# Optimization experiments

Measured on AMD Instinct MI355X. Metric: run time of the kernel, lower is better.

The kernel has to match this reference:

```python
import jax, jax.numpy as jnp
import numpy as np
from jax import lax

B, T, S = 32, 64, 400
H, E, EMB, V = 512, 1024, 256, 32000


def setup_inputs() -> dict:
    key = jax.random.key(0)
    ks = jax.random.split(key, 16)
    w = lambda k, shape: jax.random.normal(k, shape, dtype=jnp.float32) * 0.05
    return {
        "target": jax.random.randint(ks[0], (B, T), 0, V),
        "h0": jax.random.normal(ks[1], (B, H), dtype=jnp.float32),
        "c0": jax.random.normal(ks[2], (B, H), dtype=jnp.float32),
        "enc_outs": jax.random.normal(ks[3], (S, B, E), dtype=jnp.float32),
        "attn_mask": jnp.ones((B, S), dtype=jnp.int32),
        "emb": w(ks[4], (V, EMB)),
        "W_ih": w(ks[5], (4 * H, EMB)),
        "b_ih": w(ks[6], (4 * H,)),
        "W_hh": w(ks[7], (4 * H, H)),
        "b_hh": w(ks[8], (4 * H,)),
        "W_attn": w(ks[9], (H, E)),
        "b_attn": w(ks[10], (H,)),
        "W_concat": w(ks[11], (H, E + H)),
        "b_concat": w(ks[12], (H,)),
        "W_out": w(ks[13], (V, H)),
        "b_out": w(ks[14], (V,)),
    }


def reference(target, h0, c0, enc_outs, attn_mask, emb, W_ih, b_ih, W_hh, b_hh,
              W_attn, b_attn, W_concat, b_concat, W_out, b_out):
    # Precompute attention keys projection once: [S, B, H]
    keys_proj = jnp.einsum("sbe,he->sbh", enc_outs, W_attn) + b_attn
    masked = attn_mask == 0  # [B, S]
    x_seq = emb[target].transpose(1, 0, 2)  # [T, B, EMB]

    def step(carry, x_t):
        h, c = carry
        # LSTMCell (torch gate order: i, f, g, o)
        gates = x_t @ W_ih.T + b_ih + h @ W_hh.T + b_hh  # [B, 4H]
        i, f, g, o = jnp.split(gates, 4, axis=1)
        c = jax.nn.sigmoid(f) * c + jax.nn.sigmoid(i) * jnp.tanh(g)
        h = jax.nn.sigmoid(o) * jnp.tanh(c)
        # additive-style attention: sum over hidden of query*key_proj
        scores = jnp.einsum("bh,sbh->bs", h, keys_proj)  # [B, S]
        scores = jnp.where(masked, jnp.float32(-1e18), scores)
        a = jax.nn.softmax(scores, axis=1)
        ctx = jnp.einsum("bs,sbe->be", a, enc_outs)  # [B, E]
        cat = jnp.tanh(jnp.concatenate([ctx, h], axis=1) @ W_concat.T + b_concat)
        logit = jax.nn.log_softmax(cat @ W_out.T + b_out, axis=-1)  # [B, V]
        return (h, c), logit

    (_, _), logits = lax.scan(step, (h0, c0), x_seq)  # [T, B, V]
    return logits.transpose(1, 0, 2)  # [B, T, V]
```

## Files before the change

kernel.cpp:

```cpp
#include <hip/hip_runtime.h>
#include <hip/hip_bf16.h>
#include <hip/hip_fp16.h>

#define B_ 32
#define T_ 64
#define S_ 400
#define H_ 512
#define E_ 1024
#define EMB_ 256
#define V_ 32000

typedef _Float16 f16;
typedef _Float16 half8 __attribute__((ext_vector_type(8)));
typedef float f32x4 __attribute__((ext_vector_type(4)));
typedef float f32x16 __attribute__((ext_vector_type(16)));
typedef unsigned uint4v __attribute__((ext_vector_type(4)));

__device__ __forceinline__ void gl_lds16(const void* g, void* l) {
  __builtin_amdgcn_global_load_lds(
      (const __attribute__((address_space(1))) void*)g,
      (__attribute__((address_space(3))) void*)l, 16, 0, 0);
}

__device__ __forceinline__ float sigmoidf_(float x) { return 1.f / (1.f + expf(-x)); }

__device__ __forceinline__ uint4v load_b128_sys(const void* p) {
  uint4v r;
  asm volatile("global_load_dwordx4 %0, %1, off sc0 sc1" : "=v"(r) : "v"(p) : "memory");
  return r;
}
__device__ __forceinline__ void store_b128_sys(void* p, uint4v v) {
  asm volatile("global_store_dwordx4 %0, %1, off sc0 sc1" :: "v"(p), "v"(v) : "memory");
}

__global__ __launch_bounds__(256) void cvt_f16_kernel(const float* __restrict__ src,
                                                      f16* __restrict__ dst, int n2) {
  int i = blockIdx.x * 256 + threadIdx.x;
  if (i >= n2) return;
  float2 v = reinterpret_cast<const float2*>(src)[i];
  union { f16 h[2]; unsigned u; } o;
  o.h[0] = (f16)v.x; o.h[1] = (f16)v.y;
  reinterpret_cast<unsigned*>(dst)[i] = o.u;
}

__global__ __launch_bounds__(256) void gather_x_kernel(const int* __restrict__ target,
                                                       const float* __restrict__ emb,
                                                       f16* __restrict__ xin) {
  int r = blockIdx.x;
  int t = r >> 5, b = r & 31;
  int tok = target[b * T_ + t];
  xin[(size_t)r * EMB_ + threadIdx.x] = (f16)emb[(size_t)tok * EMB_ + threadIdx.x];
}

__global__ __launch_bounds__(256) void prep_kernel(const float* __restrict__ b_ih,
                                                   const float* __restrict__ b_hh,
                                                   float* __restrict__ biasperm,
                                                   const float* __restrict__ Whh,
                                                   f16* __restrict__ Wperm,
                                                   const float* __restrict__ Wih,
                                                   f16* __restrict__ Wihp,
                                                   const float* __restrict__ h0,
                                                   f16* __restrict__ hbuf) {
  int idx = blockIdx.x * 256 + threadIdx.x;
  if (idx < 4 * H_) {
    int j = idx >> 2, gg = idx & 3;
    biasperm[idx] = b_ih[gg * H_ + j] + b_hh[gg * H_ + j];
  }
  if (idx < B_ * H_) hbuf[idx] = (f16)h0[idx];
  if (idx < T_ * B_ * H_ / 8) {
    uint4v p = {0xFFFFFFFFu, 0xFFFFFFFFu, 0xFFFFFFFFu, 0xFFFFFFFFu};
    reinterpret_cast<uint4v*>(reinterpret_cast<char*>(hbuf) + (size_t)B_ * H_ * 2)[idx] = p;
  }
  {
    int j = idx >> 9, k = idx & 511;
#pragma unroll
    for (int gg = 0; gg < 4; ++gg)
      Wperm[((size_t)(j * 4 + gg)) * H_ + k] = (f16)Whh[((size_t)(gg * H_ + j)) * H_ + k];
  }
  if (idx < H_ * EMB_) {
    int j = idx >> 8, k = idx & 255;
#pragma unroll
    for (int gg = 0; gg < 4; ++gg)
      Wihp[((size_t)(j * 4 + gg)) * EMB_ + k] = (f16)Wih[((size_t)(gg * H_ + j)) * EMB_ + k];
  }
}

template <int OUTK, bool DO_TANH>
__global__ __launch_bounds__(256) void gemm_bt_kernel(const f16* __restrict__ A,
                                                      const f16* __restrict__ W,
                                                      const float* __restrict__ bias,
                                                      void* __restrict__ outp,
                                                      int M, int N, int K) {
  __shared__ __align__(16) char As[128 * 64];
  __shared__ __align__(16) char Bs[128 * 64];
  const int tid = threadIdx.x;
  const int lane = tid & 63, wave = tid >> 6;
  const int wr = (wave >> 1) * 64, wc = (wave & 1) * 64;
  const int fr = lane & 15, fq = lane >> 4;
  const int row0 = blockIdx.x * 128, col0 = blockIdx.y * 128;

  f32x4 acc[4][4];
#pragma unroll
  for (int i = 0; i < 4; ++i)
#pragma unroll
    for (int j = 0; j < 4; ++j) acc[i][j] = {0.f, 0.f, 0.f, 0.f};

  for (int k0 = 0; k0 < K; k0 += 32) {
    __syncthreads();
#pragma unroll
    for (int i = 0; i < 2; ++i) {
      int o = tid * 16 + i * 4096;
      int r = o >> 6, kk = (o & 63) >> 1;
      gl_lds16(A + (size_t)(row0 + r) * K + (k0 + kk), As + o);
      gl_lds16(W + (size_t)(col0 + r) * K + (k0 + kk), Bs + o);
    }
    __syncthreads();
    half8 af[4], bfr[4];
#pragma unroll
    for (int mi = 0; mi < 4; ++mi)
      af[mi] = *reinterpret_cast<const half8*>(As + (wr + mi * 16 + fr) * 64 + fq * 16);
#pragma unroll
    for (int ni = 0; ni < 4; ++ni)
      bfr[ni] = *reinterpret_cast<const half8*>(Bs + (wc + ni * 16 + fr) * 64 + fq * 16);
#pragma unroll
    for (int mi = 0; mi < 4; ++mi)
#pragma unroll
      for (int ni = 0; ni < 4; ++ni)
        acc[mi][ni] = __builtin_amdgcn_mfma_f32_16x16x32_f16(af[mi], bfr[ni], acc[mi][ni], 0, 0, 0);
  }

#pragma unroll
  for (int mi = 0; mi < 4; ++mi)
#pragma unroll
    for (int ni = 0; ni < 4; ++ni)
#pragma unroll
      for (int r = 0; r < 4; ++r) {
        int row = row0 + wr + mi * 16 + fq * 4 + r;
        int col = col0 + wc + ni * 16 + fr;
        float v = acc[mi][ni][r] + bias[col];
        if (DO_TANH) v = tanhf(v);
        if (OUTK == 0) {
          ((float*)outp)[(size_t)row * N + col] = v;
        } else if (OUTK == 1) {
          ((f16*)outp)[(size_t)row * N + col] = (f16)v;
        } else {
          int orow = (row & 31) * T_ + (row >> 5);
          ((float*)outp)[(size_t)orow * N + col] = v;
        }
      }
}

__global__ __launch_bounds__(512, 1) void lstm_mfma_kernel(const float* __restrict__ xpart,
                                                           const f16* __restrict__ Wperm,
                                                           const float* __restrict__ c0,
                                                           f16* __restrict__ hbuf,
                                                           f16* __restrict__ hseq,
                                                           f16* __restrict__ catin) {
  __shared__ __align__(16) char Abuf[2][32768];
  __shared__ __align__(16) f16 hstage[2][32][88];
  __shared__ int flags[8];

  const int g = blockIdx.x, tid = threadIdx.x;
  const int lane = tid & 63, wave = tid >> 6;
  const int ln31 = lane & 31, lh = lane >> 5;
  const int qq = ln31 & 3, jj = ln31 >> 2;

  if (tid < 8) flags[tid] = 0;

  half8 wf[32];
  {
    const f16* wrow = Wperm + ((size_t)(g * 256 + wave * 32 + ln31)) * H_ + lh * 8;
#pragma unroll
    for (int kc = 0; kc < 32; ++kc)
      wf[kc] = *reinterpret_cast<const half8*>(wrow + kc * 16);
  }

  const int hcol = g * 64 + wave * 8 + jj;
  float cst[4];
#pragma unroll
  for (int rg = 0; rg < 4; ++rg)
    cst[rg] = c0[(qq + 8 * rg + 4 * lh) * H_ + hcol];

  __syncthreads();

  for (int t = 0; t < T_; ++t) {
    float4 xv[4];
    {
      const float* xb = xpart + ((size_t)t * B_) * 2048 + g * 256 + wave * 32 + 4 * jj;
#pragma unroll
      for (int rg = 0; rg < 4; ++rg)
        xv[rg] = *reinterpret_cast<const float4*>(xb + (size_t)(qq + 8 * rg + 4 * lh) * 2048);
    }

    {
      int p = (t == 0) ? wave : (wave + (wave >= g ? 1 : 0));
      bool duty = (t == 0) || (wave < 7);
      if (duty) {
        const char* sb = (const char*)hbuf + (size_t)t * 32768 + ln31 * 1024 + p * 128 + lh * 16;
        while (true) {
          uint4v v0 = load_b128_sys(sb);
          uint4v v1 = load_b128_sys(sb + 32);
          uint4v v2 = load_b128_sys(sb + 64);
          uint4v v3 = load_b128_sys(sb + 96);
          asm volatile("s_waitcnt vmcnt(0)" ::: "memory");
          __builtin_amdgcn_sched_barrier(0);
          unsigned bad = 0;
#pragma unroll
          for (int d = 0; d < 4; ++d)
            bad |= (unsigned)(v0[d] == 0xFFFFFFFFu) | (unsigned)(v1[d] == 0xFFFFFFFFu) |
                   (unsigned)(v2[d] == 0xFFFFFFFFu) | (unsigned)(v3[d] == 0xFFFFFFFFu);
          if (__all(bad == 0)) {
            char* ab = Abuf[t & 1] + lane * 16;
            *(uint4v*)(ab + (size_t)(4 * p + 0) * 1024) = v0;
            *(uint4v*)(ab + (size_t)(4 * p + 1) * 1024) = v1;
            *(uint4v*)(ab + (size_t)(4 * p + 2) * 1024) = v2;
            *(uint4v*)(ab + (size_t)(4 * p + 3) * 1024) = v3;
            asm volatile("s_waitcnt lgkmcnt(0)" ::: "memory");
            __builtin_amdgcn_sched_barrier(0);
            if (lane == 0)
              __hip_atomic_store(&flags[p], t + 1, __ATOMIC_RELEASE,
                                 __HIP_MEMORY_SCOPE_WORKGROUP);
            break;
          }
        }
      }
    }

    f32x16 acA, acB;
#pragma unroll
    for (int r = 0; r < 16; ++r) { acA[r] = 0.f; acB[r] = 0.f; }
    const char* abR = Abuf[t & 1] + lane * 16;
    const f16* hsR = &hstage[(t + 1) & 1][ln31][0];
#pragma unroll
    for (int ps = 0; ps < 8; ++ps) {
      half8 a[4];
      if (ps == g && t > 0) {
#pragma unroll
        for (int c = 0; c < 4; ++c)
          a[c] = *reinterpret_cast<const half8*>(hsR + c * 16 + lh * 8);
      } else {
        while (__hip_atomic_load(&flags[ps], __ATOMIC_ACQUIRE,
                                 __HIP_MEMORY_SCOPE_WORKGROUP) < t + 1) {}
#pragma unroll
        for (int c = 0; c < 4; ++c)
          a[c] = *reinterpret_cast<const half8*>(abR + (size_t)(4 * ps + c) * 1024);
      }
      if (ps & 1) {
#pragma unroll
        for (int c = 0; c < 4; ++c)
          acB = __builtin_amdgcn_mfma_f32_32x32x16_f16(a[c], wf[4 * ps + c], acB, 0, 0, 0);
      } else {
#pragma unroll
        for (int c = 0; c < 4; ++c)
          acA = __builtin_amdgcn_mfma_f32_32x32x16_f16(a[c], wf[4 * ps + c], acA, 0, 0, 0);
      }
    }
    f32x16 acc = acA + acB;

    float u[16];
#pragma unroll
    for (int rg = 0; rg < 4; ++rg) {
      float a0 = acc[rg * 4 + 0], a1 = acc[rg * 4 + 1];
      float a2 = acc[rg * 4 + 2], a3 = acc[rg * 4 + 3];
      bool o1 = (qq & 1) != 0;
      float t01 = o1 ? a0 : a1; float r01 = __shfl_xor(t01, 1);
      a0 = o1 ? r01 : a0;  a1 = o1 ? a1 : r01;
      float t23 = o1 ? a2 : a3; float r23 = __shfl_xor(t23, 1);
      a2 = o1 ? r23 : a2;  a3 = o1 ? a3 : r23;
      bool o2 = (qq & 2) != 0;
      float t02 = o2 ? a0 : a2; float r02 = __shfl_xor(t02, 2);
      a0 = o2 ? r02 : a0;  a2 = o2 ? a2 : r02;
      float t13 = o2 ? a1 : a3; float r13 = __shfl_xor(t13, 2);
      a1 = o2 ? r13 : a1;  a3 = o2 ? a3 : r13;
      u[rg * 4 + 0] = a0; u[rg * 4 + 1] = a1; u[rg * 4 + 2] = a2; u[rg * 4 + 3] = a3;
    }

#pragma unroll
    for (int rg = 0; rg < 4; ++rg) {
      float gi = u[rg * 4 + 0] + xv[rg].x;
      float gf = u[rg * 4 + 1] + xv[rg].y;
      float gg = u[rg * 4 + 2] + xv[rg].z;
      float go = u[rg * 4 + 3] + xv[rg].w;
      float c2 = sigmoidf_(gf) * cst[rg] + sigmoidf_(gi) * tanhf(gg);
      cst[rg] = c2;
      float h = sigmoidf_(go) * tanhf(c2);
      hstage[t & 1][qq + 8 * rg + 4 * lh][wave * 8 + jj] = (f16)h;
    }
    __syncthreads();

    if (tid < 256) {
      int b = tid >> 3, c8 = tid & 7;
      uint4v v = *reinterpret_cast<const uint4v*>(&hstage[t & 1][b][c8 * 8]);
      store_b128_sys((char*)hbuf + (size_t)(t + 1) * 32768 + b * 1024 + g * 128 +
                         (c8 >> 1) * 32 + (c8 & 1) * 16,
                     v);
      *(uint4v*)((char*)hseq + ((size_t)t * B_ + b) * 1024 + g * 128 + c8 * 16) = v;
      *(uint4v*)((char*)catin + ((size_t)t * B_ + b) * 3072 + 2048 + g * 128 + c8 * 16) = v;
    }
  }
}

__global__ __launch_bounds__(64) void scores_kernel(const f16* __restrict__ hseq,
                                                    const f16* __restrict__ keys,
                                                    float* __restrict__ attnw) {
  int s = blockIdx.x, b = blockIdx.y;
  int t = threadIdx.x;
  const half8* hv = reinterpret_cast<const half8*>(hseq + ((size_t)t * B_ + b) * H_);
  const half8* kv = reinterpret_cast<const half8*>(keys + ((size_t)s * B_ + b) * H_);
  float acc = 0.f;
#pragma unroll 4
  for (int k = 0; k < H_ / 8; ++k) {
    half8 a = hv[k], c = kv[k];
#pragma unroll
    for (int i = 0; i < 8; ++i) acc += (float)a[i] * (float)c[i];
  }
  attnw[((size_t)b * S_ + s) * T_ + t] = acc;
}

__global__ __launch_bounds__(64) void softmax_kernel(float* __restrict__ attnw,
                                                     const int* __restrict__ mask) {
  int b = blockIdx.x, t = blockIdx.y, l = threadIdx.x;
  float vals[7];
  float m = -3.4e38f;
#pragma unroll
  for (int i = 0; i < 7; ++i) {
    int s = l + i * 64;
    float v = -3.4e38f;
    if (s < S_) {
      v = attnw[((size_t)b * S_ + s) * T_ + t];
      if (mask[b * S_ + s] == 0) v = -1e18f;
    }
    vals[i] = v;
    m = fmaxf(m, v);
  }
#pragma unroll
  for (int o = 32; o > 0; o >>= 1) m = fmaxf(m, __shfl_xor(m, o));
  float sum = 0.f;
#pragma unroll
  for (int i = 0; i < 7; ++i) {
    int s = l + i * 64;
    if (s < S_) { float e = expf(vals[i] - m); vals[i] = e; sum += e; }
  }
#pragma unroll
  for (int o = 32; o > 0; o >>= 1) sum += __shfl_xor(sum, o);
  float inv = 1.f / sum;
#pragma unroll
  for (int i = 0; i < 7; ++i) {
    int s = l + i * 64;
    if (s < S_) attnw[((size_t)b * S_ + s) * T_ + t] = vals[i] * inv;
  }
}

__global__ __launch_bounds__(256) void ctx_kernel(const float* __restrict__ attnw,
                                                  const f16* __restrict__ enc,
                                                  f16* __restrict__ catin) {
  int b = blockIdx.x, e0 = blockIdx.y * 64;
  int el = threadIdx.x & 63, tq = threadIdx.x >> 6;
  __shared__ float a_lds[100 * 64];
  float acc[16];
#pragma unroll
  for (int i = 0; i < 16; ++i) acc[i] = 0.f;
  for (int sc = 0; sc < 4; ++sc) {
    __syncthreads();
    for (int i = threadIdx.x; i < 6400; i += 256)
      a_lds[i] = attnw[((size_t)b * S_ + sc * 100) * T_ + i];
    __syncthreads();
    for (int sl = 0; sl < 100; ++sl) {
      int s = sc * 100 + sl;
      float v = (float)enc[((size_t)s * B_ + b) * E_ + e0 + el];
#pragma unroll
      for (int i = 0; i < 16; ++i) acc[i] += a_lds[sl * 64 + tq * 16 + i] * v;
    }
  }
#pragma unroll
  for (int i = 0; i < 16; ++i) {
    int t = tq * 16 + i;
    catin[((size_t)t * B_ + b) * (E_ + H_) + e0 + el] = (f16)acc[i];
  }
}

__global__ __launch_bounds__(512, 1) void logsm_kernel(float* __restrict__ out) {
  int r = blockIdx.x;
  size_t base = (size_t)r * V_;
  int tid = threadIdx.x;
  float4* op = reinterpret_cast<float4*>(out + base);
  float4 v[16];
  float m = -3.4e38f;
#pragma unroll
  for (int k = 0; k < 16; ++k) {
    int c = tid + (k << 9);
    if (c < 8000) {
      v[k] = op[c];
      m = fmaxf(m, fmaxf(fmaxf(v[k].x, v[k].y), fmaxf(v[k].z, v[k].w)));
    }
  }
  __shared__ float red[8];
#pragma unroll
  for (int o = 32; o > 0; o >>= 1) m = fmaxf(m, __shfl_xor(m, o));
  if ((tid & 63) == 0) red[tid >> 6] = m;
  __syncthreads();
  float mm = red[0];
#pragma unroll
  for (int i = 1; i < 8; ++i) mm = fmaxf(mm, red[i]);
  float s = 0.f;
#pragma unroll
  for (int k = 0; k < 16; ++k) {
    int c = tid + (k << 9);
    if (c < 8000)
      s += expf(v[k].x - mm) + expf(v[k].y - mm) + expf(v[k].z - mm) + expf(v[k].w - mm);
  }
#pragma unroll
  for (int o = 32; o > 0; o >>= 1) s += __shfl_xor(s, o);
  __syncthreads();
  if ((tid & 63) == 0) red[tid >> 6] = s;
  __syncthreads();
  s = 0.f;
#pragma unroll
  for (int i = 0; i < 8; ++i) s += red[i];
  float lse = mm + logf(s);
#pragma unroll
  for (int k = 0; k < 16; ++k) {
    int c = tid + (k << 9);
    if (c < 8000) {
      float4 o4;
      o4.x = v[k].x - lse; o4.y = v[k].y - lse;
      o4.z = v[k].z - lse; o4.w = v[k].w - lse;
      op[c] = o4;
    }
  }
}

extern "C" void kernel_launch(void* const* d_in, const int* in_sizes, int n_in,
                              void* d_out, int out_size, void* d_ws, size_t ws_size,
                              hipStream_t stream) {
  const int*   target = (const int*)d_in[0];
  const float* h0     = (const float*)d_in[1];
  const float* c0     = (const float*)d_in[2];
  const float* enc    = (const float*)d_in[3];
  const int*   mask   = (const int*)d_in[4];
  const float* emb    = (const float*)d_in[5];
  const float* W_ih   = (const float*)d_in[6];
  const float* b_ih   = (const float*)d_in[7];
  const float* W_hh   = (const float*)d_in[8];
  const float* b_hh   = (const float*)d_in[9];
  const float* W_attn = (const float*)d_in[10];
  const float* b_attn = (const float*)d_in[11];
  const float* W_cat  = (const float*)d_in[12];
  const float* b_cat  = (const float*)d_in[13];
  const float* W_out  = (const float*)d_in[14];
  const float* b_out  = (const float*)d_in[15];

  char* ws = (char*)d_ws;
  size_t off = 0;
  auto alloc = [&](size_t bytes) {
    void* p = ws + off;
    off = (off + bytes + 255) & ~(size_t)255;
    return p;
  };
  f16*   enc_f    = (f16*)alloc((size_t)S_ * B_ * E_ * 2);
  f16*   keys_f   = (f16*)alloc((size_t)S_ * B_ * H_ * 2);
  f16*   Wattn_f  = (f16*)alloc((size_t)H_ * E_ * 2);
  f16*   Wcat_f   = (f16*)alloc((size_t)H_ * (E_ + H_) * 2);
  f16*   Wout_f   = (f16*)alloc((size_t)V_ * H_ * 2);
  f16*   Wperm    = (f16*)alloc((size_t)4 * H_ * H_ * 2);
  f16*   Wihp     = (f16*)alloc((size_t)4 * H_ * EMB_ * 2);
  float* biasperm = (float*)alloc((size_t)4 * H_ * 4);
  f16*   xin_f    = (f16*)alloc((size_t)T_ * B_ * EMB_ * 2);
  float* xpart    = (float*)alloc((size_t)T_ * B_ * 4 * H_ * 4);
  f16*   hseq_f   = (f16*)alloc((size_t)T_ * B_ * H_ * 2);
  f16*   catin_f  = (f16*)alloc((size_t)T_ * B_ * (E_ + H_) * 2);
  float* attnw    = (float*)alloc((size_t)B_ * S_ * T_ * 4);
  f16*   catbuf_f = (f16*)alloc((size_t)T_ * B_ * H_ * 2);
  f16*   hbuf     = (f16*)alloc((size_t)(T_ + 1) * B_ * H_ * 2);
  (void)ws_size; (void)in_sizes; (void)n_in; (void)out_size;

  auto cvt = [&](const float* s, f16* d, size_t n) {
    int n2 = (int)(n / 2);
    cvt_f16_kernel<<<(n2 + 255) / 256, 256, 0, stream>>>(s, d, n2);
  };
  cvt(enc, enc_f, (size_t)S_ * B_ * E_);
  cvt(W_attn, Wattn_f, (size_t)H_ * E_);
  cvt(W_cat, Wcat_f, (size_t)H_ * (E_ + H_));
  cvt(W_out, Wout_f, (size_t)V_ * H_);
  gather_x_kernel<<<T_ * B_, 256, 0, stream>>>(target, emb, xin_f);
  prep_kernel<<<(H_ * H_) / 256, 256, 0, stream>>>(b_ih, b_hh, biasperm, W_hh, Wperm,
                                                   W_ih, Wihp, h0, hbuf);

  gemm_bt_kernel<1, false><<<dim3((S_ * B_) / 128, H_ / 128), 256, 0, stream>>>(
      enc_f, Wattn_f, b_attn, keys_f, S_ * B_, H_, E_);
  gemm_bt_kernel<0, false><<<dim3((T_ * B_) / 128, (4 * H_) / 128), 256, 0, stream>>>(
      xin_f, Wihp, biasperm, xpart, T_ * B_, 4 * H_, EMB_);

  lstm_mfma_kernel<<<8, 512, 0, stream>>>(xpart, Wperm, c0, hbuf, hseq_f, catin_f);

  scores_kernel<<<dim3(S_, B_), 64, 0, stream>>>(hseq_f, keys_f, attnw);
  softmax_kernel<<<dim3(B_, T_), 64, 0, stream>>>(attnw, mask);
  ctx_kernel<<<dim3(B_, E_ / 64), 256, 0, stream>>>(attnw, enc_f, catin_f);

  gemm_bt_kernel<1, true><<<dim3((T_ * B_) / 128, H_ / 128), 256, 0, stream>>>(
      catin_f, Wcat_f, b_cat, catbuf_f, T_ * B_, H_, E_ + H_);
  gemm_bt_kernel<2, false><<<dim3((T_ * B_) / 128, V_ / 128), 256, 0, stream>>>(
      catbuf_f, Wout_f, b_out, (float*)d_out, T_ * B_, V_, H_);

  logsm_kernel<<<B_ * T_, 512, 0, stream>>>((float*)d_out);
}
```

Measured before the change: 887.4 us.

## Remove block barrier from LSTM step via per-wave h publishing

```diff
diff --git a/kernel.cpp b/kernel.cpp
--- a/kernel.cpp
+++ b/kernel.cpp
@@ -153,11 +153,9 @@
 __global__ __launch_bounds__(512, 1) void lstm_mfma_kernel(const float* __restrict__ xpart,
                                                            const f16* __restrict__ Wperm,
                                                            const float* __restrict__ c0,
-                                                           f16* __restrict__ hbuf,
-                                                           f16* __restrict__ hseq,
-                                                           f16* __restrict__ catin) {
+                                                           f16* __restrict__ hbuf) {
   __shared__ __align__(16) char Abuf[2][32768];
-  __shared__ __align__(16) f16 hstage[2][32][88];
+  __shared__ __align__(16) f16 wavepack[8][32][8];
   __shared__ int flags[8];
 
   const int g = blockIdx.x, tid = threadIdx.x;
@@ -193,35 +191,32 @@
     }
 
     {
-      int p = (t == 0) ? wave : (wave + (wave >= g ? 1 : 0));
-      bool duty = (t == 0) || (wave < 7);
-      if (duty) {
-        const char* sb = (const char*)hbuf + (size_t)t * 32768 + ln31 * 1024 + p * 128 + lh * 16;
-        while (true) {
-          uint4v v0 = load_b128_sys(sb);
-          uint4v v1 = load_b128_sys(sb + 32);
-          uint4v v2 = load_b128_sys(sb + 64);
-          uint4v v3 = load_b128_sys(sb + 96);
-          asm volatile("s_waitcnt vmcnt(0)" ::: "memory");
+      const int p = wave;
+      const char* sb = (const char*)hbuf + (size_t)t * 32768 + ln31 * 1024 + p * 128 + lh * 16;
+      while (true) {
+        uint4v v0 = load_b128_sys(sb);
+        uint4v v1 = load_b128_sys(sb + 32);
+        uint4v v2 = load_b128_sys(sb + 64);
+        uint4v v3 = load_b128_sys(sb + 96);
+        asm volatile("s_waitcnt vmcnt(0)" ::: "memory");
+        __builtin_amdgcn_sched_barrier(0);
+        unsigned bad = 0;
+#pragma unroll
+        for (int d = 0; d < 4; ++d)
+          bad |= (unsigned)(v0[d] == 0xFFFFFFFFu) | (unsigned)(v1[d] == 0xFFFFFFFFu) |
+                 (unsigned)(v2[d] == 0xFFFFFFFFu) | (unsigned)(v3[d] == 0xFFFFFFFFu);
+        if (__all(bad == 0)) {
+          char* ab = Abuf[t & 1] + lane * 16;
+          *(uint4v*)(ab + (size_t)(4 * p + 0) * 1024) = v0;
+          *(uint4v*)(ab + (size_t)(4 * p + 1) * 1024) = v1;
+          *(uint4v*)(ab + (size_t)(4 * p + 2) * 1024) = v2;
+          *(uint4v*)(ab + (size_t)(4 * p + 3) * 1024) = v3;
+          asm volatile("s_waitcnt lgkmcnt(0)" ::: "memory");
           __builtin_amdgcn_sched_barrier(0);
-          unsigned bad = 0;
-#pragma unroll
-          for (int d = 0; d < 4; ++d)
-            bad |= (unsigned)(v0[d] == 0xFFFFFFFFu) | (unsigned)(v1[d] == 0xFFFFFFFFu) |
-                   (unsigned)(v2[d] == 0xFFFFFFFFu) | (unsigned)(v3[d] == 0xFFFFFFFFu);
-          if (__all(bad == 0)) {
-            char* ab = Abuf[t & 1] + lane * 16;
-            *(uint4v*)(ab + (size_t)(4 * p + 0) * 1024) = v0;
-            *(uint4v*)(ab + (size_t)(4 * p + 1) * 1024) = v1;
-            *(uint4v*)(ab + (size_t)(4 * p + 2) * 1024) = v2;
-            *(uint4v*)(ab + (size_t)(4 * p + 3) * 1024) = v3;
-            asm volatile("s_waitcnt lgkmcnt(0)" ::: "memory");
-            __builtin_amdgcn_sched_barrier(0);
-            if (lane == 0)
-              __hip_atomic_store(&flags[p], t + 1, __ATOMIC_RELEASE,
-                                 __HIP_MEMORY_SCOPE_WORKGROUP);
-            break;
-          }
+          if (lane == 0)
+            __hip_atomic_store(&flags[p], t + 1, __ATOMIC_RELEASE,
+                               __HIP_MEMORY_SCOPE_WORKGROUP);
+          break;
         }
       }
     }
@@ -230,21 +225,14 @@
 #pragma unroll
     for (int r = 0; r < 16; ++r) { acA[r] = 0.f; acB[r] = 0.f; }
     const char* abR = Abuf[t & 1] + lane * 16;
-    const f16* hsR = &hstage[(t + 1) & 1][ln31][0];
 #pragma unroll
     for (int ps = 0; ps < 8; ++ps) {
+      while (__hip_atomic_load(&flags[ps], __ATOMIC_ACQUIRE,
+                               __HIP_MEMORY_SCOPE_WORKGROUP) < t + 1) {}
       half8 a[4];
-      if (ps == g && t > 0) {
-#pragma unroll
-        for (int c = 0; c < 4; ++c)
-          a[c] = *reinterpret_cast<const half8*>(hsR + c * 16 + lh * 8);
-      } else {
-        while (__hip_atomic_load(&flags[ps], __ATOMIC_ACQUIRE,
-                                 __HIP_MEMORY_SCOPE_WORKGROUP) < t + 1) {}
-#pragma unroll
-        for (int c = 0; c < 4; ++c)
-          a[c] = *reinterpret_cast<const half8*>(abR + (size_t)(4 * ps + c) * 1024);
-      }
+#pragma unroll
+      for (int c = 0; c < 4; ++c)
+        a[c] = *reinterpret_cast<const half8*>(abR + (size_t)(4 * ps + c) * 1024);
       if (ps & 1) {
 #pragma unroll
         for (int c = 0; c < 4; ++c)
@@ -284,20 +272,25 @@
       float c2 = sigmoidf_(gf) * cst[rg] + sigmoidf_(gi) * tanhf(gg);
       cst[rg] = c2;
       float h = sigmoidf_(go) * tanhf(c2);
-      hstage[t & 1][qq + 8 * rg + 4 * lh][wave * 8 + jj] = (f16)h;
-    }
-    __syncthreads();
-
-    if (tid < 256) {
-      int b = tid >> 3, c8 = tid & 7;
-      uint4v v = *reinterpret_cast<const uint4v*>(&hstage[t & 1][b][c8 * 8]);
-      store_b128_sys((char*)hbuf + (size_t)(t + 1) * 32768 + b * 1024 + g * 128 +
-                         (c8 >> 1) * 32 + (c8 & 1) * 16,
+      wavepack[wave][qq + 8 * rg + 4 * lh][jj] = (f16)h;
+    }
+    asm volatile("s_waitcnt lgkmcnt(0)" ::: "memory");
+    __builtin_amdgcn_sched_barrier(0);
+
+    if (lh == 0) {
+      uint4v v = *reinterpret_cast<const uint4v*>(&wavepack[wave][ln31][0]);
+      store_b128_sys((char*)hbuf + (size_t)(t + 1) * 32768 + ln31 * 1024 + g * 128 + wave * 16,
                      v);
-      *(uint4v*)((char*)hseq + ((size_t)t * B_ + b) * 1024 + g * 128 + c8 * 16) = v;
-      *(uint4v*)((char*)catin + ((size_t)t * B_ + b) * 3072 + 2048 + g * 128 + c8 * 16) = v;
-    }
-  }
+    }
+  }
+}
+
+__global__ __launch_bounds__(128) void catcopy_kernel(const f16* __restrict__ hseq,
+                                                      f16* __restrict__ catin) {
+  int r = blockIdx.x;
+  const uint2* src = reinterpret_cast<const uint2*>(hseq + (size_t)r * H_);
+  uint2* dst = reinterpret_cast<uint2*>(catin + (size_t)r * (E_ + H_) + E_);
+  dst[threadIdx.x] = src[threadIdx.x];
 }
 
 __global__ __launch_bounds__(64) void scores_kernel(const f16* __restrict__ hseq,
@@ -467,12 +460,13 @@
   float* biasperm = (float*)alloc((size_t)4 * H_ * 4);
   f16*   xin_f    = (f16*)alloc((size_t)T_ * B_ * EMB_ * 2);
   float* xpart    = (float*)alloc((size_t)T_ * B_ * 4 * H_ * 4);
-  f16*   hseq_f   = (f16*)alloc((size_t)T_ * B_ * H_ * 2);
   f16*   catin_f  = (f16*)alloc((size_t)T_ * B_ * (E_ + H_) * 2);
   float* attnw    = (float*)alloc((size_t)B_ * S_ * T_ * 4);
   f16*   catbuf_f = (f16*)alloc((size_t)T_ * B_ * H_ * 2);
   f16*   hbuf     = (f16*)alloc((size_t)(T_ + 1) * B_ * H_ * 2);
   (void)ws_size; (void)in_sizes; (void)n_in; (void)out_size;
+
+  f16* hseq_f = hbuf + (size_t)B_ * H_;
 
   auto cvt = [&](const float* s, f16* d, size_t n) {
     int n2 = (int)(n / 2);
@@ -491,8 +485,9 @@
   gemm_bt_kernel<0, false><<<dim3((T_ * B_) / 128, (4 * H_) / 128), 256, 0, stream>>>(
       xin_f, Wihp, biasperm, xpart, T_ * B_, 4 * H_, EMB_);
 
-  lstm_mfma_kernel<<<8, 512, 0, stream>>>(xpart, Wperm, c0, hbuf, hseq_f, catin_f);
-
+  lstm_mfma_kernel<<<8, 512, 0, stream>>>(xpart, Wperm, c0, hbuf);
+
+  catcopy_kernel<<<T_ * B_, 128, 0, stream>>>(hseq_f, catin_f);
   scores_kernel<<<dim3(S_, B_), 64, 0, stream>>>(hseq_f, keys_f, attnw);
   softmax_kernel<<<dim3(B_, T_), 64, 0, stream>>>(attnw, mask);
   ctx_kernel<<<dim3(B_, E_ / 64), 256, 0, stream>>>(attnw, enc_f, catin_f);
```

After: 928.6 us. 4.6% more time.
